# Optimization experiments

Measured on AMD Instinct MI355X. Metric: run time of the kernel, lower is better.

## Reference

```python
import jax, jax.numpy as jnp
import numpy as np

ALPHA = 9.0
EPS = 2.220446049250313e-16  # sys.float_info.epsilon
N, K = 131072, 256


def setup_inputs() -> dict:
    key = jax.random.key(0)
    k1, k2 = jax.random.split(key)
    latent_view_1 = jax.random.uniform(k1, (N, K), dtype=jnp.float32)
    latent_view_2 = jax.random.uniform(k2, (N, K), dtype=jnp.float32)
    return {"latent_view_1": latent_view_1, "latent_view_2": latent_view_2}


def reference(latent_view_1, latent_view_2):
    # joint: sum_n v1[n,i] * v2[n,j]  == v1^T @ v2  (rank-N GEMM, [k,k] output)
    p_i_j = jnp.einsum('ni,nj->ij', latent_view_1, latent_view_2)
    p_i_j = (p_i_j + p_i_j.T) / 2.0
    p_i_j = p_i_j / jnp.sum(p_i_j)
    p_i = jnp.sum(p_i_j, axis=1, keepdims=True)  # [k,1] marginal
    p_j = jnp.sum(p_i_j, axis=0, keepdims=True)  # [1,k] marginal
    p_i_j = jnp.maximum(p_i_j, EPS)
    p_i = jnp.maximum(p_i, EPS)
    p_j = jnp.maximum(p_j, EPS)
    loss = -p_i_j * (jnp.log(p_i_j)
                     - (ALPHA + 1.0) * jnp.log(p_j)
                     - (ALPHA + 1.0) * jnp.log(p_i))
    return jnp.sum(loss)
```

## Files before the change

kernel.cpp:

```cpp
#include <hip/hip_runtime.h>
#include <hip/hip_bf16.h>

#define KDIM 256
#define NTOT 131072
#define PN   65536
#define NB   256
#define RPB  512
#define CHROWS 16
#define CH   (CHROWS*KDIM)
#define NTL  16
#define EPSF 2.220446049250313e-16f

typedef float f32x4 __attribute__((ext_vector_type(4)));
typedef __bf16 bf16x8 __attribute__((ext_vector_type(8)));
typedef unsigned short u16x8 __attribute__((ext_vector_type(8)));

__device__ __forceinline__ unsigned short f2bf(float x){
  unsigned u = __float_as_uint(x);
  u += 0x7fffu + ((u >> 16) & 1u);
  return (unsigned short)(u >> 16);
}
__device__ __forceinline__ unsigned pk2(float lo, float hi){
  return (unsigned)f2bf(lo) | ((unsigned)f2bf(hi) << 16);
}
__device__ __forceinline__ float bf2f(unsigned short u){
  return __uint_as_float((unsigned)u << 16);
}
__device__ __forceinline__ int swz(int i){ return (((i >> 1) ^ (i >> 4)) & 7) << 4; }

struct Stage { f32x4 r0, r1; };

__device__ __forceinline__ void stage_load(Stage& s, const float* src, long off){
  s.r0 = *(const f32x4*)(src + off);
  s.r1 = *(const f32x4*)(src + off + KDIM);
}

__device__ __forceinline__ void stage_store(const Stage& s, char* tile, const int* offW){
#pragma unroll
  for (int m = 0; m < 4; ++m)
    *(unsigned*)(tile + offW[m]) = pk2(s.r0[m], s.r1[m]);
}

__device__ __forceinline__ void compute_t(const char* As, const char* Bs,
                                          const int* offA, const int* offB,
                                          f32x4 (&acc)[4][4])
{
  bf16x8 af[4], bfr[4];
#pragma unroll
  for (int m = 0; m < 4; ++m) af[m]  = *(const bf16x8*)(As + offA[m]);
#pragma unroll
  for (int n = 0; n < 4; ++n) bfr[n] = *(const bf16x8*)(Bs + offB[n]);
#pragma unroll
  for (int m = 0; m < 4; ++m)
#pragma unroll
    for (int n = 0; n < 4; ++n)
      acc[m][n] = __builtin_amdgcn_mfma_f32_16x16x32_bf16(af[m], bfr[n], acc[m][n], 0, 0, 0);
}

__device__ __forceinline__ void lds_fence_barrier(){
  __builtin_amdgcn_sched_barrier(0);
  asm volatile("s_waitcnt lgkmcnt(0)");
  __builtin_amdgcn_sched_barrier(0);
  __builtin_amdgcn_s_barrier();
  __builtin_amdgcn_sched_barrier(0);
}

__global__ __launch_bounds__(1024) void k_gemm(const float* __restrict__ v1,
                                               const float* __restrict__ v2,
                                               unsigned short* __restrict__ part,
                                               float* __restrict__ csum)
{
  __shared__ char sm[65536];
  const int t    = threadIdx.x;
  const int b    = blockIdx.x;
  if (b == 0 && t < 256) csum[t] = 0.f;
  const int lane = t & 63, wid = t >> 6;
  const int di   = lane & 15, g = lane >> 4;
  const int wr   = wid >> 2, wc = wid & 3;
  const int i0   = wr * 64, j0 = wc * 64;

  const int mtx = t >> 9;
  const int p   = t & 7;
  const int q   = (t >> 3) & 63;
  const float* src = (mtx ? v2 : v1) + ((long)b * RPB + 2 * p) * KDIM + 4 * q;
  const int sbase = mtx * 16384;

  int offW0[4], offW1[4], offA[4], offB[4];
#pragma unroll
  for (int m = 0; m < 4; ++m){
    const int i   = 4*q + m;
    const int lin = (i << 6) + (p << 2);
    offW0[m] = sbase + ( lin        ^ swz(i));
    offW1[m] = sbase + ((lin + 32)  ^ swz(i));
  }
#pragma unroll
  for (int m = 0; m < 4; ++m){ int i = i0 + 16*m + di; offA[m] = ((i << 6) + (g << 4)) ^ swz(i); }
#pragma unroll
  for (int n = 0; n < 4; ++n){ int j = j0 + 16*n + di; offB[n] = ((j << 6) + (g << 4)) ^ swz(j); }

  f32x4 acc[4][4];
#pragma unroll
  for (int m = 0; m < 4; ++m)
#pragma unroll
    for (int n = 0; n < 4; ++n){ f32x4 z = {0.f,0.f,0.f,0.f}; acc[m][n] = z; }

  Stage S0, S1;
  stage_load(S0, src, 0L * CH);
  stage_load(S1, src, 1L * CH);
  stage_store(S0, sm, offW0);
  __builtin_amdgcn_sched_barrier(0);
  stage_load(S0, src, 2L * CH);
  __builtin_amdgcn_sched_barrier(0);
  stage_store(S1, sm, offW1);
  __builtin_amdgcn_sched_barrier(0);
  stage_load(S1, src, 3L * CH);
  lds_fence_barrier();

#pragma unroll 2
  for (int it = 0; it < NTL - 2; ++it){
    char* Tc = sm + (it & 1) * 32768;
    char* Tn = sm + ((it + 1) & 1) * 32768;
    stage_store(S0, Tn, offW0);
    __builtin_amdgcn_sched_barrier(0);
    stage_load(S0, src, (long)(2*it + 4) * CH);
    __builtin_amdgcn_sched_barrier(0);
    stage_store(S1, Tn, offW1);
    __builtin_amdgcn_sched_barrier(0);
    stage_load(S1, src, (long)(2*it + 5) * CH);
    __builtin_amdgcn_sched_barrier(0);
    compute_t(Tc, Tc + 16384, offA, offB, acc);
    lds_fence_barrier();
  }

  {
    char* Tc = sm + ((NTL - 2) & 1) * 32768;
    char* Tn = sm + ((NTL - 1) & 1) * 32768;
    stage_store(S0, Tn, offW0);
    stage_store(S1, Tn, offW1);
    __builtin_amdgcn_sched_barrier(0);
    compute_t(Tc, Tc + 16384, offA, offB, acc);
    lds_fence_barrier();
    compute_t(Tn, Tn + 16384, offA, offB, acc);
  }

  unsigned short* op = part + (size_t)b * PN;
#pragma unroll
  for (int m = 0; m < 4; ++m)
#pragma unroll
    for (int n = 0; n < 4; ++n){
      const int i = i0 + 16*m + 4*g;
      const int j = j0 + 16*n + di;
#pragma unroll
      for (int r = 0; r < 4; ++r)
        op[(size_t)(i + r) * KDIM + j] = f2bf(acc[m][n][r]);
    }
}

__global__ __launch_bounds__(1024) void k_reduce(const unsigned short* __restrict__ part,
                                                 float* __restrict__ P,
                                                 float* __restrict__ rsum,
                                                 float* __restrict__ csum,
                                                 float* __restrict__ out)
{
  __shared__ float red[32][288];
  const int gr = blockIdx.x;
  const int t  = threadIdx.x;
  const int q  = t >> 5;
  const int o  = t & 31;
  float a[8];
#pragma unroll
  for (int e = 0; e < 8; ++e) a[e] = 0.f;
  const unsigned short* p = part + (size_t)(q * 8) * PN + gr * KDIM + o * 8;
#pragma unroll
  for (int k = 0; k < 8; ++k){
    const u16x8 u = *(const u16x8*)(p + (size_t)k * PN);
#pragma unroll
    for (int e = 0; e < 8; ++e) a[e] += bf2f(u[e]);
  }
#pragma unroll
  for (int e = 0; e < 8; ++e) red[q][o * 9 + e] = a[e];
  __syncthreads();
  float v = 0.f;
  if (t < 256){
    const int idx = (t >> 3) * 9 + (t & 7);
#pragma unroll
    for (int g = 0; g < 32; ++g) v += red[g][idx];
    P[gr * KDIM + t] = v;
    atomicAdd(&csum[t], v);
  }
  __syncthreads();
  if (t < 256) red[0][t] = v;
  __syncthreads();
  for (int st = 128; st > 0; st >>= 1){
    if (t < st) red[0][t] += red[0][t + st];
    __syncthreads();
  }
  if (t == 0){
    rsum[gr] = red[0][0];
    if (gr == 0) out[0] = 0.f;
  }
}

__global__ __launch_bounds__(256) void k_loss(const float* __restrict__ P,
                                              const float* __restrict__ rsum,
                                              const float* __restrict__ csum,
                                              float* __restrict__ out)
{
  __shared__ float lm[256];
  __shared__ float red[256];
  const int t = threadIdx.x;
  const float ri = rsum[t];
  red[t] = ri; __syncthreads();
  for (int st = 128; st > 0; st >>= 1){
    if (t < st) red[t] += red[t + st];
    __syncthreads();
  }
  const float S = red[0];
  const float inv2S = 0.5f / S;
  lm[t] = logf(fmaxf((ri + csum[t]) * inv2S, EPSF));
  __syncthreads();

  float acc = 0.f;
  const int base = blockIdx.x * 512;
#pragma unroll
  for (int e = base + t; e < base + 512; e += 256){
    const int i = e >> 8, j = e & 255;
    float qv = (P[i * KDIM + j] + P[j * KDIM + i]) * inv2S;
    qv = fmaxf(qv, EPSF);
    acc += -qv * (logf(qv) - 10.0f * (lm[i] + lm[j]));
  }
  red[t] = acc; __syncthreads();
  for (int st = 128; st > 0; st >>= 1){
    if (t < st) red[t] += red[t + st];
    __syncthreads();
  }
  if (t == 0) atomicAdd(out, red[0]);
}

extern "C" void kernel_launch(void* const* d_in, const int* in_sizes, int n_in,
                              void* d_out, int out_size, void* d_ws, size_t ws_size,
                              hipStream_t stream) {
  const float* v1 = (const float*)d_in[0];
  const float* v2 = (const float*)d_in[1];
  float* out = (float*)d_out;
  char*  wsc = (char*)d_ws;

  unsigned short* part = (unsigned short*)wsc;
  float* P    = (float*)(wsc + (size_t)NB * PN * 2);
  float* rsum = P + PN;
  float* csum = rsum + 256;

  k_gemm  <<<NB, 1024, 0, stream>>>(v1, v2, part, csum);
  k_reduce<<<256, 1024, 0, stream>>>(part, P, rsum, csum, out);
  k_loss  <<<128, 256, 0, stream>>>(P, rsum, csum, out);
}
```

Measured before the change: 71.19 us.

## Fuse GEMM, reduce and loss kernels into one cooperative kernel with grid barriers

```diff
diff --git a/kernel.cpp b/kernel.cpp
--- a/kernel.cpp
+++ b/kernel.cpp
@@ -65,176 +65,179 @@
   __builtin_amdgcn_sched_barrier(0);
 }
 
-__global__ __launch_bounds__(1024) void k_gemm(const float* __restrict__ v1,
-                                               const float* __restrict__ v2,
-                                               unsigned short* __restrict__ part,
-                                               float* __restrict__ csum)
+__device__ __forceinline__ void grid_barrier(unsigned* cnt, unsigned target){
+  __syncthreads();
+  if (threadIdx.x == 0){
+    __threadfence();
+    __hip_atomic_fetch_add(cnt, 1u, __ATOMIC_RELEASE, __HIP_MEMORY_SCOPE_AGENT);
+    while (__hip_atomic_load(cnt, __ATOMIC_ACQUIRE, __HIP_MEMORY_SCOPE_AGENT) < target)
+      __builtin_amdgcn_s_sleep(2);
+  }
+  __syncthreads();
+}
+
+__global__ __launch_bounds__(1024) void k_fused(const float* __restrict__ v1,
+                                                const float* __restrict__ v2,
+                                                unsigned short* __restrict__ part,
+                                                float* __restrict__ P,
+                                                float* __restrict__ rsum,
+                                                float* __restrict__ csum,
+                                                unsigned* __restrict__ cnt,
+                                                float* __restrict__ out)
 {
   __shared__ char sm[65536];
   const int t    = threadIdx.x;
   const int b    = blockIdx.x;
-  if (b == 0 && t < 256) csum[t] = 0.f;
-  const int lane = t & 63, wid = t >> 6;
-  const int di   = lane & 15, g = lane >> 4;
-  const int wr   = wid >> 2, wc = wid & 3;
-  const int i0   = wr * 64, j0 = wc * 64;
-
-  const int mtx = t >> 9;
-  const int p   = t & 7;
-  const int q   = (t >> 3) & 63;
-  const float* src = (mtx ? v2 : v1) + ((long)b * RPB + 2 * p) * KDIM + 4 * q;
-  const int sbase = mtx * 16384;
-
-  int offW0[4], offW1[4], offA[4], offB[4];
-#pragma unroll
-  for (int m = 0; m < 4; ++m){
-    const int i   = 4*q + m;
-    const int lin = (i << 6) + (p << 2);
-    offW0[m] = sbase + ( lin        ^ swz(i));
-    offW1[m] = sbase + ((lin + 32)  ^ swz(i));
-  }
-#pragma unroll
-  for (int m = 0; m < 4; ++m){ int i = i0 + 16*m + di; offA[m] = ((i << 6) + (g << 4)) ^ swz(i); }
-#pragma unroll
-  for (int n = 0; n < 4; ++n){ int j = j0 + 16*n + di; offB[n] = ((j << 6) + (g << 4)) ^ swz(j); }
-
-  f32x4 acc[4][4];
-#pragma unroll
-  for (int m = 0; m < 4; ++m)
-#pragma unroll
-    for (int n = 0; n < 4; ++n){ f32x4 z = {0.f,0.f,0.f,0.f}; acc[m][n] = z; }
-
-  Stage S0, S1;
-  stage_load(S0, src, 0L * CH);
-  stage_load(S1, src, 1L * CH);
-  stage_store(S0, sm, offW0);
-  __builtin_amdgcn_sched_barrier(0);
-  stage_load(S0, src, 2L * CH);
-  __builtin_amdgcn_sched_barrier(0);
-  stage_store(S1, sm, offW1);
-  __builtin_amdgcn_sched_barrier(0);
-  stage_load(S1, src, 3L * CH);
-  lds_fence_barrier();
+
+  {
+    if (b == 0 && t < 256) csum[t] = 0.f;
+    const int lane = t & 63, wid = t >> 6;
+    const int di   = lane & 15, g = lane >> 4;
+    const int wr   = wid >> 2, wc = wid & 3;
+    const int i0   = wr * 64, j0 = wc * 64;
+
+    const int mtx = t >> 9;
+    const int p   = t & 7;
+    const int q   = (t >> 3) & 63;
+    const float* src = (mtx ? v2 : v1) + ((long)b * RPB + 2 * p) * KDIM + 4 * q;
+    const int sbase = mtx * 16384;
+
+    int offW0[4], offW1[4], offA[4], offB[4];
+#pragma unroll
+    for (int m = 0; m < 4; ++m){
+      const int i   = 4*q + m;
+      const int lin = (i << 6) + (p << 2);
+      offW0[m] = sbase + ( lin        ^ swz(i));
+      offW1[m] = sbase + ((lin + 32)  ^ swz(i));
+    }
+#pragma unroll
+    for (int m = 0; m < 4; ++m){ int i = i0 + 16*m + di; offA[m] = ((i << 6) + (g << 4)) ^ swz(i); }
+#pragma unroll
+    for (int n = 0; n < 4; ++n){ int j = j0 + 16*n + di; offB[n] = ((j << 6) + (g << 4)) ^ swz(j); }
+
+    f32x4 acc[4][4];
+#pragma unroll
+    for (int m = 0; m < 4; ++m)
+#pragma unroll
+      for (int n = 0; n < 4; ++n){ f32x4 z = {0.f,0.f,0.f,0.f}; acc[m][n] = z; }
+
+    Stage S0, S1;
+    stage_load(S0, src, 0L * CH);
+    stage_load(S1, src, 1L * CH);
+    stage_store(S0, sm, offW0);
+    __builtin_amdgcn_sched_barrier(0);
+    stage_load(S0, src, 2L * CH);
+    __builtin_amdgcn_sched_barrier(0);
+    stage_store(S1, sm, offW1);
+    __builtin_amdgcn_sched_barrier(0);
+    stage_load(S1, src, 3L * CH);
+    lds_fence_barrier();
 
 #pragma unroll 2
-  for (int it = 0; it < NTL - 2; ++it){
-    char* Tc = sm + (it & 1) * 32768;
-    char* Tn = sm + ((it + 1) & 1) * 32768;
-    stage_store(S0, Tn, offW0);
-    __builtin_amdgcn_sched_barrier(0);
-    stage_load(S0, src, (long)(2*it + 4) * CH);
-    __builtin_amdgcn_sched_barrier(0);
-    stage_store(S1, Tn, offW1);
-    __builtin_amdgcn_sched_barrier(0);
-    stage_load(S1, src, (long)(2*it + 5) * CH);
-    __builtin_amdgcn_sched_barrier(0);
-    compute_t(Tc, Tc + 16384, offA, offB, acc);
-    lds_fence_barrier();
-  }
+    for (int it = 0; it < NTL - 2; ++it){
+      char* Tc = sm + (it & 1) * 32768;
+      char* Tn = sm + ((it + 1) & 1) * 32768;
+      stage_store(S0, Tn, offW0);
+      __builtin_amdgcn_sched_barrier(0);
+      stage_load(S0, src, (long)(2*it + 4) * CH);
+      __builtin_amdgcn_sched_barrier(0);
+      stage_store(S1, Tn, offW1);
+      __builtin_amdgcn_sched_barrier(0);
+      stage_load(S1, src, (long)(2*it + 5) * CH);
+      __builtin_amdgcn_sched_barrier(0);
+      compute_t(Tc, Tc + 16384, offA, offB, acc);
+      lds_fence_barrier();
+    }
+    {
+      char* Tc = sm + ((NTL - 2) & 1) * 32768;
+      char* Tn = sm + ((NTL - 1) & 1) * 32768;
+      stage_store(S0, Tn, offW0);
+      stage_store(S1, Tn, offW1);
+      __builtin_amdgcn_sched_barrier(0);
+      compute_t(Tc, Tc + 16384, offA, offB, acc);
+      lds_fence_barrier();
+      compute_t(Tn, Tn + 16384, offA, offB, acc);
+    }
+
+    unsigned short* op = part + (size_t)b * PN;
+#pragma unroll
+    for (int m = 0; m < 4; ++m)
+#pragma unroll
+      for (int n = 0; n < 4; ++n){
+        const int i = i0 + 16*m + 4*g;
+        const int j = j0 + 16*n + di;
+#pragma unroll
+        for (int r = 0; r < 4; ++r)
+          op[(size_t)(i + r) * KDIM + j] = f2bf(acc[m][n][r]);
+      }
+  }
+
+  grid_barrier(cnt + 0, NB);
+  if (b == 0 && t == 0) out[0] = 0.f;
 
   {
-    char* Tc = sm + ((NTL - 2) & 1) * 32768;
-    char* Tn = sm + ((NTL - 1) & 1) * 32768;
-    stage_store(S0, Tn, offW0);
-    stage_store(S1, Tn, offW1);
-    __builtin_amdgcn_sched_barrier(0);
-    compute_t(Tc, Tc + 16384, offA, offB, acc);
-    lds_fence_barrier();
-    compute_t(Tn, Tn + 16384, offA, offB, acc);
-  }
-
-  unsigned short* op = part + (size_t)b * PN;
-#pragma unroll
-  for (int m = 0; m < 4; ++m)
-#pragma unroll
-    for (int n = 0; n < 4; ++n){
-      const int i = i0 + 16*m + 4*g;
-      const int j = j0 + 16*n + di;
-#pragma unroll
-      for (int r = 0; r < 4; ++r)
-        op[(size_t)(i + r) * KDIM + j] = f2bf(acc[m][n][r]);
-    }
-}
-
-__global__ __launch_bounds__(1024) void k_reduce(const unsigned short* __restrict__ part,
-                                                 float* __restrict__ P,
-                                                 float* __restrict__ rsum,
-                                                 float* __restrict__ csum,
-                                                 float* __restrict__ out)
-{
-  __shared__ float red[32][288];
-  const int gr = blockIdx.x;
-  const int t  = threadIdx.x;
-  const int q  = t >> 5;
-  const int o  = t & 31;
-  float a[8];
-#pragma unroll
-  for (int e = 0; e < 8; ++e) a[e] = 0.f;
-  const unsigned short* p = part + (size_t)(q * 8) * PN + gr * KDIM + o * 8;
-#pragma unroll
-  for (int k = 0; k < 8; ++k){
-    const u16x8 u = *(const u16x8*)(p + (size_t)k * PN);
-#pragma unroll
-    for (int e = 0; e < 8; ++e) a[e] += bf2f(u[e]);
-  }
-#pragma unroll
-  for (int e = 0; e < 8; ++e) red[q][o * 9 + e] = a[e];
-  __syncthreads();
-  float v = 0.f;
-  if (t < 256){
-    const int idx = (t >> 3) * 9 + (t & 7);
-#pragma unroll
-    for (int g = 0; g < 32; ++g) v += red[g][idx];
-    P[gr * KDIM + t] = v;
-    atomicAdd(&csum[t], v);
-  }
-  __syncthreads();
-  if (t < 256) red[0][t] = v;
-  __syncthreads();
-  for (int st = 128; st > 0; st >>= 1){
-    if (t < st) red[0][t] += red[0][t + st];
-    __syncthreads();
-  }
-  if (t == 0){
-    rsum[gr] = red[0][0];
-    if (gr == 0) out[0] = 0.f;
-  }
-}
-
-__global__ __launch_bounds__(256) void k_loss(const float* __restrict__ P,
-                                              const float* __restrict__ rsum,
-                                              const float* __restrict__ csum,
-                                              float* __restrict__ out)
-{
-  __shared__ float lm[256];
-  __shared__ float red[256];
-  const int t = threadIdx.x;
-  const float ri = rsum[t];
-  red[t] = ri; __syncthreads();
-  for (int st = 128; st > 0; st >>= 1){
-    if (t < st) red[t] += red[t + st];
-    __syncthreads();
-  }
-  const float S = red[0];
-  const float inv2S = 0.5f / S;
-  lm[t] = logf(fmaxf((ri + csum[t]) * inv2S, EPSF));
-  __syncthreads();
-
-  float acc = 0.f;
-  const int base = blockIdx.x * 512;
-#pragma unroll
-  for (int e = base + t; e < base + 512; e += 256){
-    const int i = e >> 8, j = e & 255;
-    float qv = (P[i * KDIM + j] + P[j * KDIM + i]) * inv2S;
-    qv = fmaxf(qv, EPSF);
-    acc += -qv * (logf(qv) - 10.0f * (lm[i] + lm[j]));
-  }
-  red[t] = acc; __syncthreads();
-  for (int st = 128; st > 0; st >>= 1){
-    if (t < st) red[t] += red[t + st];
-    __syncthreads();
-  }
-  if (t == 0) atomicAdd(out, red[0]);
+    float (*red)[288] = (float(*)[288])sm;
+    const int q = t >> 5;
+    const int o = t & 31;
+    float a[8];
+#pragma unroll
+    for (int e = 0; e < 8; ++e) a[e] = 0.f;
+    const unsigned short* p = part + (size_t)(q * 8) * PN + b * KDIM + o * 8;
+#pragma unroll
+    for (int k = 0; k < 8; ++k){
+      const u16x8 u = *(const u16x8*)(p + (size_t)k * PN);
+#pragma unroll
+      for (int e = 0; e < 8; ++e) a[e] += bf2f(u[e]);
+    }
+#pragma unroll
+    for (int e = 0; e < 8; ++e) red[q][o * 9 + e] = a[e];
+    __syncthreads();
+    float v = 0.f;
+    if (t < 256){
+      const int idx = (t >> 3) * 9 + (t & 7);
+#pragma unroll
+      for (int g2 = 0; g2 < 32; ++g2) v += red[g2][idx];
+      P[b * KDIM + t] = v;
+      atomicAdd(&csum[t], v);
+    }
+    __syncthreads();
+    if (t < 256) red[0][t] = v;
+    __syncthreads();
+    for (int st = 128; st > 0; st >>= 1){
+      if (t < st) red[0][t] += red[0][t + st];
+      __syncthreads();
+    }
+    if (t == 0) rsum[b] = red[0][0];
+  }
+
+  grid_barrier(cnt + 1, NB);
+
+  {
+    float* lmp = (float*)sm;
+    float* rd  = lmp + 256;
+    float ri = 0.f;
+    if (t < 256){ ri = rsum[t]; rd[t] = ri; }
+    __syncthreads();
+    for (int st = 128; st > 0; st >>= 1){
+      if (t < st) rd[t] += rd[t + st];
+      __syncthreads();
+    }
+    const float S = rd[0];
+    const float inv2S = 0.5f / S;
+    __syncthreads();
+    if (t < 256) lmp[t] = logf(fmaxf((ri + csum[t]) * inv2S, EPSF));
+    __syncthreads();
+    if (t < 256){
+      const float qv = fmaxf((P[b * KDIM + t] + P[t * KDIM + b]) * inv2S, EPSF);
+      rd[t] = -qv * (logf(qv) - 10.0f * (lmp[b] + lmp[t]));
+    }
+    __syncthreads();
+    for (int st = 128; st > 0; st >>= 1){
+      if (t < st) rd[t] += rd[t + st];
+      __syncthreads();
+    }
+    if (t == 0) atomicAdd(out, rd[0]);
+  }
 }
 
 extern "C" void kernel_launch(void* const* d_in, const int* in_sizes, int n_in,
@@ -249,8 +252,11 @@
   float* P    = (float*)(wsc + (size_t)NB * PN * 2);
   float* rsum = P + PN;
   float* csum = rsum + 256;
-
-  k_gemm  <<<NB, 1024, 0, stream>>>(v1, v2, part, csum);
-  k_reduce<<<256, 1024, 0, stream>>>(part, P, rsum, csum, out);
-  k_loss  <<<128, 256, 0, stream>>>(P, rsum, csum, out);
-}
+  unsigned* cnt = (unsigned*)(csum + 256);
+
+  hipMemsetAsync(cnt, 0, 2 * sizeof(unsigned), stream);
+  void* args[] = {(void*)&v1, (void*)&v2, (void*)&part, (void*)&P,
+                  (void*)&rsum, (void*)&csum, (void*)&cnt, (void*)&out};
+  hipLaunchCooperativeKernel(reinterpret_cast<void*>(k_fused),
+                             dim3(NB), dim3(1024), args, 0, stream);
+}
```

After: 153.2 us. +115.2%, slower.

## Fuse reduce and loss kernels using a last-block-done atomic counter

Applied to the files above, without the earlier changes.

```diff
diff --git a/kernel.cpp b/kernel.cpp
--- a/kernel.cpp
+++ b/kernel.cpp
@@ -156,85 +156,96 @@
     }
 }
 
-__global__ __launch_bounds__(1024) void k_reduce(const unsigned short* __restrict__ part,
-                                                 float* __restrict__ P,
-                                                 float* __restrict__ rsum,
-                                                 float* __restrict__ csum,
-                                                 float* __restrict__ out)
+__global__ __launch_bounds__(1024) void k_redloss(const unsigned short* __restrict__ part,
+                                                  float* __restrict__ P,
+                                                  float* __restrict__ rsum,
+                                                  float* __restrict__ csum,
+                                                  unsigned* __restrict__ cnt,
+                                                  float* __restrict__ out)
 {
   __shared__ float red[32][288];
+  __shared__ int lastf;
   const int gr = blockIdx.x;
   const int t  = threadIdx.x;
-  const int q  = t >> 5;
-  const int o  = t & 31;
-  float a[8];
-#pragma unroll
-  for (int e = 0; e < 8; ++e) a[e] = 0.f;
-  const unsigned short* p = part + (size_t)(q * 8) * PN + gr * KDIM + o * 8;
-#pragma unroll
-  for (int k = 0; k < 8; ++k){
-    const u16x8 u = *(const u16x8*)(p + (size_t)k * PN);
-#pragma unroll
-    for (int e = 0; e < 8; ++e) a[e] += bf2f(u[e]);
-  }
-#pragma unroll
-  for (int e = 0; e < 8; ++e) red[q][o * 9 + e] = a[e];
-  __syncthreads();
-  float v = 0.f;
-  if (t < 256){
-    const int idx = (t >> 3) * 9 + (t & 7);
-#pragma unroll
-    for (int g = 0; g < 32; ++g) v += red[g][idx];
-    P[gr * KDIM + t] = v;
-    atomicAdd(&csum[t], v);
-  }
-  __syncthreads();
-  if (t < 256) red[0][t] = v;
+
+  {
+    const int q = t >> 5;
+    const int o = t & 31;
+    float a[8];
+#pragma unroll
+    for (int e = 0; e < 8; ++e) a[e] = 0.f;
+    const unsigned short* p = part + (size_t)(q * 8) * PN + gr * KDIM + o * 8;
+#pragma unroll
+    for (int k = 0; k < 8; ++k){
+      const u16x8 u = *(const u16x8*)(p + (size_t)k * PN);
+#pragma unroll
+      for (int e = 0; e < 8; ++e) a[e] += bf2f(u[e]);
+    }
+#pragma unroll
+    for (int e = 0; e < 8; ++e) red[q][o * 9 + e] = a[e];
+    __syncthreads();
+    float v = 0.f;
+    if (t < 256){
+      const int idx = (t >> 3) * 9 + (t & 7);
+#pragma unroll
+      for (int g2 = 0; g2 < 32; ++g2) v += red[g2][idx];
+      P[gr * KDIM + t] = v;
+      atomicAdd(&csum[t], v);
+    }
+    __syncthreads();
+    if (t < 256) red[0][t] = v;
+    __syncthreads();
+    for (int st = 128; st > 0; st >>= 1){
+      if (t < st) red[0][t] += red[0][t + st];
+      __syncthreads();
+    }
+    if (t == 0) rsum[gr] = red[0][0];
+  }
+
+  __syncthreads();
+  if (t == 0){
+    __threadfence();
+    const unsigned prev = __hip_atomic_fetch_add(cnt, 1u, __ATOMIC_ACQ_REL,
+                                                 __HIP_MEMORY_SCOPE_AGENT);
+    lastf = (prev == NB - 1);
+  }
+  __syncthreads();
+  if (!lastf) return;
+  __threadfence();
+  __syncthreads();
+
+  float* flat = &red[0][0];
+  float* lm = flat;
+  float* rd = flat + 256;
+  float ri = 0.f;
+  if (t < 256){ ri = rsum[t]; rd[t] = ri; }
   __syncthreads();
   for (int st = 128; st > 0; st >>= 1){
-    if (t < st) red[0][t] += red[0][t + st];
-    __syncthreads();
-  }
-  if (t == 0){
-    rsum[gr] = red[0][0];
-    if (gr == 0) out[0] = 0.f;
-  }
-}
-
-__global__ __launch_bounds__(256) void k_loss(const float* __restrict__ P,
-                                              const float* __restrict__ rsum,
-                                              const float* __restrict__ csum,
-                                              float* __restrict__ out)
-{
-  __shared__ float lm[256];
-  __shared__ float red[256];
-  const int t = threadIdx.x;
-  const float ri = rsum[t];
-  red[t] = ri; __syncthreads();
-  for (int st = 128; st > 0; st >>= 1){
-    if (t < st) red[t] += red[t + st];
-    __syncthreads();
-  }
-  const float S = red[0];
+    if (t < st) rd[t] += rd[t + st];
+    __syncthreads();
+  }
+  const float S = rd[0];
   const float inv2S = 0.5f / S;
-  lm[t] = logf(fmaxf((ri + csum[t]) * inv2S, EPSF));
+  __syncthreads();
+  if (t < 256) lm[t] = logf(fmaxf((ri + csum[t]) * inv2S, EPSF));
   __syncthreads();
 
   float acc = 0.f;
-  const int base = blockIdx.x * 512;
-#pragma unroll
-  for (int e = base + t; e < base + 512; e += 256){
+#pragma unroll
+  for (int e = t; e < PN; e += 1024){
     const int i = e >> 8, j = e & 255;
     float qv = (P[i * KDIM + j] + P[j * KDIM + i]) * inv2S;
     qv = fmaxf(qv, EPSF);
     acc += -qv * (logf(qv) - 10.0f * (lm[i] + lm[j]));
   }
-  red[t] = acc; __syncthreads();
-  for (int st = 128; st > 0; st >>= 1){
-    if (t < st) red[t] += red[t + st];
-    __syncthreads();
-  }
-  if (t == 0) atomicAdd(out, red[0]);
+  __syncthreads();
+  flat[t] = acc;
+  __syncthreads();
+  for (int st = 512; st > 0; st >>= 1){
+    if (t < st) flat[t] += flat[t + st];
+    __syncthreads();
+  }
+  if (t == 0) out[0] = flat[0];
 }
 
 extern "C" void kernel_launch(void* const* d_in, const int* in_sizes, int n_in,
@@ -249,8 +260,9 @@
   float* P    = (float*)(wsc + (size_t)NB * PN * 2);
   float* rsum = P + PN;
   float* csum = rsum + 256;
-
-  k_gemm  <<<NB, 1024, 0, stream>>>(v1, v2, part, csum);
-  k_reduce<<<256, 1024, 0, stream>>>(part, P, rsum, csum, out);
-  k_loss  <<<128, 256, 0, stream>>>(P, rsum, csum, out);
-}
+  unsigned* cnt = (unsigned*)(csum + 256);
+
+  hipMemsetAsync(cnt, 0, sizeof(unsigned), stream);
+  k_gemm   <<<NB, 1024, 0, stream>>>(v1, v2, part, csum);
+  k_redloss<<<NB, 1024, 0, stream>>>(part, P, rsum, csum, cnt, out);
+}
```

New measurement: 132.3 us. 1.86x slower.
